# Kernel optimization log

Hardware: AMD Instinct MI355X
Metric: run time of the kernel (lower is better)

The kernel has to match this reference:

```python
import jax, jax.numpy as jnp
import numpy as np
from jax import lax

K = 3  # neighbors, as in torch_geometric.nn.knn_interpolate default
EPS = 1e-16


def knn_interpolate(x, pos_x, pos_y):
    """Interpolate features x defined at pos_x onto query points pos_y.
    x: [Ns, F], pos_x: [Ns, 3], pos_y: [Nq, 3] -> [Nq, F].
    Inverse squared-distance weighting over K nearest neighbors."""
    # squared distances via the |y|^2 + |x|^2 - 2 y.x expansion (no [Nq,Ns,3] temp)
    d2 = (jnp.sum(pos_y * pos_y, -1, keepdims=True)
          + jnp.sum(pos_x * pos_x, -1)[None, :]
          - 2.0 * pos_y @ pos_x.T)                      # [Nq, Ns]
    neg_d2, idx = lax.top_k(-d2, K)                      # [Nq, K]
    w = 1.0 / jnp.clip(-neg_d2, EPS)                     # inverse squared distance
    w = w / jnp.sum(w, -1, keepdims=True)
    return jnp.einsum('qk,qkf->qf', w, x[idx])           # gather + weighted reduce


def mlp(x, W1, b1, W2, b2, W3, b3):
    x = jax.nn.relu(x @ W1 + b1)
    x = jax.nn.relu(x @ W2 + b2)
    return x @ W3 + b3


def setup_inputs() -> dict:
    key = jax.random.key(0)
    ks = jax.random.split(key, 16)
    Nh, Nl, H, O = 16384, 4096, 256, 3
    s = lambda fan: 1.0 / np.sqrt(fan)
    return {
        'emb1':  jax.random.normal(ks[0], (Nh, H), jnp.float32),
        'l_y1':  jax.random.normal(ks[1], (Nl, O), jnp.float32),
        'l_pos1': jax.random.uniform(ks[2], (Nl, 3), jnp.float32),
        'h_pos1': jax.random.uniform(ks[3], (Nh, 3), jnp.float32),
        'emb2':  jax.random.normal(ks[4], (Nh, H), jnp.float32),
        'l_y2':  jax.random.normal(ks[5], (Nl, O), jnp.float32),
        'l_pos2': jax.random.uniform(ks[6], (Nl, 3), jnp.float32),
        'h_pos2': jax.random.uniform(ks[7], (Nh, 3), jnp.float32),
        'W1': jax.random.uniform(ks[8], (H, H), jnp.float32, -s(H), s(H)),
        'b1': jax.random.uniform(ks[9], (H,), jnp.float32, -s(H), s(H)),
        'W2': jax.random.uniform(ks[10], (H, H), jnp.float32, -s(H), s(H)),
        'b2': jax.random.uniform(ks[11], (H,), jnp.float32, -s(H), s(H)),
        'W3': jax.random.uniform(ks[12], (H, O), jnp.float32, -s(H), s(H)),
        'b3': jax.random.uniform(ks[13], (O,), jnp.float32, -s(H), s(H)),
    }


def reference(emb1, l_y1, l_pos1, h_pos1, emb2, l_y2, l_pos2, h_pos2,
              W1, b1, W2, b2, W3, b3):
    x = mlp(emb1 - knn_interpolate(emb2, h_pos2, h_pos1), W1, b1, W2, b2, W3, b3)
    # residual=True branch
    res = knn_interpolate(l_y1 - knn_interpolate(l_y2, l_pos2, l_pos1), l_pos1, h_pos1)
    return x + res
```

## Files before the change

### kernel.cpp

```cpp
#include <hip/hip_runtime.h>
#include <math.h>

#define BIGF 3.0e38f

typedef short  s16x8 __attribute__((ext_vector_type(8)));
typedef float  f32x4 __attribute__((ext_vector_type(4)));

__device__ __forceinline__ unsigned short f2bf(float x) {
  unsigned int b = __float_as_uint(x);
  unsigned int r = b + 0x7FFFu + ((b >> 16) & 1u);
  return (unsigned short)(r >> 16);
}
__device__ __forceinline__ float bf2f(unsigned short h) {
  return __uint_as_float(((unsigned int)h) << 16);
}


__device__ __forceinline__ int cell_clamp(float v, int G) {
  int c = (int)(v * (float)G);
  return min(G - 1, max(0, c));
}

__device__ __forceinline__ void ins3(float d, int id,
                                     float& d0, float& d1, float& d2,
                                     int& i0, int& i1, int& i2) {
  bool l0 = (d < d0) || (d == d0 && id < i0);
  bool l1 = (d < d1) || (d == d1 && id < i1);
  bool l2 = (d < d2) || (d == d2 && id < i2);
  float nd0 = l0 ? d  : d0;  int ni0 = l0 ? id : i0;
  float nd1 = l0 ? d0 : (l1 ? d  : d1);
  int   ni1 = l0 ? i0 : (l1 ? id : i1);
  float nd2 = l1 ? d1 : (l2 ? d  : d2);
  int   ni2 = l1 ? i1 : (l2 ? id : i2);
  d0 = nd0; d1 = nd1; d2 = nd2; i0 = ni0; i1 = ni1; i2 = ni2;
}

__device__ void knn_body(
    int bid,
    const float4* __restrict__ qspts, const int* __restrict__ qsidx, int Nq, int G,
    const int* __restrict__ offs,
    const float4* __restrict__ spts,
    const int* __restrict__ sidx,
    int mode,
    const float* __restrict__ base3,
    const float* __restrict__ feat3,
    float* __restrict__ w_out, int* __restrict__ i_out,
    float* __restrict__ out3)
{
  #pragma clang fp contract(off)
  const int sl = threadIdx.x & 15;
  const int qs = bid * 16 + (threadIdx.x >> 4);
  if (qs >= Nq) return;

  float4 qv = qspts[qs];
  const float qx = qv.x, qy = qv.y, qz = qv.z;
  const float sy = qv.w;
  const int qorig = qsidx[qs];
  const float cs = 1.0f / (float)G;
  const int cx = cell_clamp(qx, G), cy = cell_clamp(qy, G), cz = cell_clamp(qz, G);

  float d0 = BIGF, d1 = BIGF, d2v = BIGF;
  int i0 = -1, i1 = -1, i2 = -1;
  float e0 = BIGF, e1 = BIGF, e2 = BIGF;
  int j0 = -1, j1 = -1, j2 = -1;
  bool done = false;

  #define SCAN()                                                              \
    for (int j = js; j < je; ++j) {                                           \
      float4 s = spts[j];                                                     \
      float p0 = qx * s.x, p1 = qy * s.y, p2 = qz * s.z;                      \
      float dt = (p0 + p1) + p2;                                              \
      float S  = sy + s.w;                                                    \
      float dd = S - 2.0f * dt;                                               \
      ins3(dd, sidx[j], d0, d1, d2v, i0, i1, i2);                             \
    }

  for (int R = 1; R <= G; ++R) {
    if (!done) {
      if (R == 1) {
        if (sl < 9) {
          int dy = sl % 3 - 1, dz = sl / 3 - 1;
          int yy = cy + dy, zz = cz + dz;
          if (yy >= 0 && yy < G && zz >= 0 && zz < G) {
            int xs = max(cx - 1, 0), xe = min(cx + 1, G - 1);
            int base = (zz * G + yy) * G;
            int js = offs[base + xs], je = offs[base + xe + 1];
            SCAN()
          }
        }
      } else {
        const int twoR1 = 2 * R + 1, inner = 2 * R - 1;
        const int nfz = 2 * twoR1;
        const int nfull = nfz + 2 * inner;
        const int half = inner * inner;
        const int nitems = nfull + 2 * half;
        for (int m = sl; m < nitems; m += 16) {
          int dy, dz, js, je;
          if (m < nfull) {
            if (m < nfz) { dz = (m < twoR1) ? -R : R; dy = (m % twoR1) - R; }
            else { int u = m - nfz; dy = (u < inner) ? -R : R; dz = (u % inner) - (R - 1); }
            int yy = cy + dy, zz = cz + dz;
            if (yy < 0 || yy >= G || zz < 0 || zz >= G) continue;
            int xs = max(cx - R, 0), xe = min(cx + R, G - 1);
            int base = (zz * G + yy) * G;
            js = offs[base + xs]; je = offs[base + xe + 1];
          } else {
            int u = m - nfull;
            int xc = (u < half) ? (cx - R) : (cx + R);
            int r2 = (u < half) ? u : u - half;
            dy = r2 % inner - (R - 1); dz = r2 / inner - (R - 1);
            int yy = cy + dy, zz = cz + dz;
            if (xc < 0 || xc >= G || yy < 0 || yy >= G || zz < 0 || zz >= G) continue;
            int c = (zz * G + yy) * G + xc;
            js = offs[c]; je = offs[c + 1];
          }
          SCAN()
        }
      }
    }
    e0 = d0; e1 = d1; e2 = d2v; j0 = i0; j1 = i1; j2 = i2;
    #pragma unroll
    for (int msk = 1; msk < 16; msk <<= 1) {
      float o0 = __shfl_xor(e0, msk), o1 = __shfl_xor(e1, msk), o2 = __shfl_xor(e2, msk);
      int   p0 = __shfl_xor(j0, msk), p1 = __shfl_xor(j1, msk), p2 = __shfl_xor(j2, msk);
      ins3(o0, p0, e0, e1, e2, j0, j1, j2);
      ins3(o1, p1, e0, e1, e2, j0, j1, j2);
      ins3(o2, p2, e0, e1, e2, j0, j1, j2);
    }
    float bnd = (float)R * cs;
    done = done || (e2 <= bnd * bnd - 1e-6f);
    if (__all(done)) break;
  }
  #undef SCAN

  if (sl == 0) {
    float w0 = 1.0f / fmaxf(e0, 1e-16f);
    float w1 = 1.0f / fmaxf(e1, 1e-16f);
    float w2 = 1.0f / fmaxf(e2, 1e-16f);
    float inv = 1.0f / (w0 + w1 + w2);
    w0 *= inv; w1 *= inv; w2 *= inv;
    if (mode == 0) {
      w_out[(size_t)qorig * 3 + 0] = w0; w_out[(size_t)qorig * 3 + 1] = w1; w_out[(size_t)qorig * 3 + 2] = w2;
      i_out[(size_t)qorig * 3 + 0] = j0; i_out[(size_t)qorig * 3 + 1] = j1; i_out[(size_t)qorig * 3 + 2] = j2;
    } else {
      #pragma unroll
      for (int f = 0; f < 3; ++f) {
        float v = w0 * feat3[(size_t)j0 * 3 + f]
                + w1 * feat3[(size_t)j1 * 3 + f]
                + w2 * feat3[(size_t)j2 * 3 + f];
        out3[(size_t)qorig * 3 + f] = (mode == 1) ? (base3[(size_t)qorig * 3 + f] - v) : v;
      }
    }
  }
}

__device__ void build_t_body(
    int bid, const float* __restrict__ emb1, const float* __restrict__ emb2,
    const float* __restrict__ w, const int* __restrict__ idx,
    unsigned short* __restrict__ t_hi, unsigned short* __restrict__ t_lo, int Nq)
{
  int gid = bid * 256 + threadIdx.x;
  int q = gid >> 6, c4 = gid & 63;
  if (q >= Nq) return;
  float w0 = w[(size_t)q * 3 + 0], w1 = w[(size_t)q * 3 + 1], w2 = w[(size_t)q * 3 + 2];
  int i0 = idx[(size_t)q * 3 + 0], i1 = idx[(size_t)q * 3 + 1], i2 = idx[(size_t)q * 3 + 2];
  const float4* e1 = (const float4*)emb1;
  const float4* e2 = (const float4*)emb2;
  float4 a  = e1[(size_t)q * 64 + c4];
  float4 f0 = e2[(size_t)i0 * 64 + c4];
  float4 f1 = e2[(size_t)i1 * 64 + c4];
  float4 f2 = e2[(size_t)i2 * 64 + c4];
  float4 r;
  r.x = a.x - (w0 * f0.x + w1 * f1.x + w2 * f2.x);
  r.y = a.y - (w0 * f0.y + w1 * f1.y + w2 * f2.y);
  r.z = a.z - (w0 * f0.z + w1 * f1.z + w2 * f2.z);
  r.w = a.w - (w0 * f0.w + w1 * f1.w + w2 * f2.w);
  ushort4 h, l;
  h.x = f2bf(r.x); l.x = f2bf(r.x - bf2f(h.x));
  h.y = f2bf(r.y); l.y = f2bf(r.y - bf2f(h.y));
  h.z = f2bf(r.z); l.z = f2bf(r.z - bf2f(h.z));
  h.w = f2bf(r.w); l.w = f2bf(r.w - bf2f(h.w));
  size_t o = (size_t)q * 256 + c4 * 4;
  *(ushort4*)&t_hi[o] = h;
  *(ushort4*)&t_lo[o] = l;
}

__device__ void res_gather_body(
    int bid, const float* __restrict__ wC, const int* __restrict__ idxC,
    const float* __restrict__ diff, float* __restrict__ res, int Nq)
{
  int q = bid * 256 + threadIdx.x;
  if (q >= Nq) return;
  float w0 = wC[(size_t)q * 3 + 0], w1 = wC[(size_t)q * 3 + 1], w2 = wC[(size_t)q * 3 + 2];
  int i0 = idxC[(size_t)q * 3 + 0], i1 = idxC[(size_t)q * 3 + 1], i2 = idxC[(size_t)q * 3 + 2];
  #pragma unroll
  for (int f = 0; f < 3; ++f) {
    res[(size_t)q * 3 + f] = w0 * diff[(size_t)i0 * 3 + f]
                           + w1 * diff[(size_t)i1 * 3 + f]
                           + w2 * diff[(size_t)i2 * 3 + f];
  }
}

__global__ __launch_bounds__(256) void knn_triple_kernel(
    const float4* qspts, const int* qsidx, int Nh, int G1,
    const int* offs1, const float4* spts1, const int* sidx1, float* wA, int* idxA,
    const float4* spts3, const int* sidx3, int Nl, int G2,
    const int* offs2, const float4* spts2, const int* sidx2,
    const float* l_y1, const float* l_y2, float* diff,
    const int* offs3, float* wC, int* idxC)
{
  int g = blockIdx.x / 9, r = blockIdx.x % 9;
  if (r < 4)
    knn_body(g * 4 + r, qspts, qsidx, Nh, G1, offs1, spts1, sidx1, 0,
             nullptr, nullptr, wA, idxA, nullptr);
  else if (r == 4)
    knn_body(g, spts3, sidx3, Nl, G2, offs2, spts2, sidx2, 1,
             l_y1, l_y2, nullptr, nullptr, diff);
  else
    knn_body(g * 4 + (r - 5), qspts, qsidx, Nh, G2, offs3, spts3, sidx3, 0,
             nullptr, nullptr, wC, idxC, nullptr);
}

__global__ __launch_bounds__(256) void bt_gather_kernel(
    const float* emb1, const float* emb2, const float* w, const int* idx,
    unsigned short* t_hi, unsigned short* t_lo, int Nq_bt,
    const float* wC, const int* idxC, const float* diff, float* res, int NqG)
{
  if (blockIdx.x < 64)
    res_gather_body(blockIdx.x, wC, idxC, diff, res, NqG);
  else
    build_t_body(blockIdx.x - 64, emb1, emb2, w, idx, t_hi, t_lo, Nq_bt);
}

__global__ __launch_bounds__(256) void zero_kernel(int* __restrict__ p, int n) {
  int i = blockIdx.x * 256 + threadIdx.x;
  if (i < n) p[i] = 0;
}

__global__ __launch_bounds__(256) void cell_count4_kernel(
    const float* __restrict__ p1, int n1, int g1, int* __restrict__ c1,
    const float* __restrict__ p2, int n2, int g2, int* __restrict__ c2,
    const float* __restrict__ p3, int n3, int g3, int* __restrict__ c3,
    const float* __restrict__ p4, int n4, int g4, int* __restrict__ c4)
{
  int b = blockIdx.x;
  const float* p; int n, G; int* cnt; int i;
  if (b < 64)       { p = p1; n = n1; G = g1; cnt = c1; i = b * 256 + threadIdx.x; }
  else if (b < 80)  { p = p2; n = n2; G = g2; cnt = c2; i = (b - 64) * 256 + threadIdx.x; }
  else if (b < 96)  { p = p3; n = n3; G = g3; cnt = c3; i = (b - 80) * 256 + threadIdx.x; }
  else              { p = p4; n = n4; G = g4; cnt = c4; i = (b - 96) * 256 + threadIdx.x; }
  if (i >= n) return;
  int cx = cell_clamp(p[3 * i],     G);
  int cy = cell_clamp(p[3 * i + 1], G);
  int cz = cell_clamp(p[3 * i + 2], G);
  atomicAdd(&cnt[(cz * G + cy) * G + cx], 1);
}

__global__ __launch_bounds__(256) void prefix4_kernel(
    const int* __restrict__ c1, int* __restrict__ o1, int* __restrict__ u1, int m1,
    const int* __restrict__ c2, int* __restrict__ o2, int* __restrict__ u2, int m2,
    const int* __restrict__ c3, int* __restrict__ o3, int* __restrict__ u3, int m3,
    const int* __restrict__ c4, int* __restrict__ o4, int* __restrict__ u4, int m4)
{
  const int* cnt; int* offs; int* cur; int M;
  if (blockIdx.x == 0)      { cnt = c1; offs = o1; cur = u1; M = m1; }
  else if (blockIdx.x == 1) { cnt = c2; offs = o2; cur = u2; M = m2; }
  else if (blockIdx.x == 2) { cnt = c3; offs = o3; cur = u3; M = m3; }
  else                      { cnt = c4; offs = o4; cur = u4; M = m4; }
  __shared__ int ps[256];
  const int tid = threadIdx.x;
  const int per = (M + 255) >> 8;
  const int base = tid * per;
  int s = 0;
  for (int j = 0; j < per; ++j) if (base + j < M) s += cnt[base + j];
  ps[tid] = s;
  __syncthreads();
  for (int off = 1; off < 256; off <<= 1) {
    int v = (tid >= off) ? ps[tid - off] : 0;
    __syncthreads();
    ps[tid] += v;
    __syncthreads();
  }
  int run = (tid > 0) ? ps[tid - 1] : 0;
  for (int j = 0; j < per; ++j) {
    if (base + j < M) {
      offs[base + j] = run; cur[base + j] = run;
      run += cnt[base + j];
    }
  }
  if (tid == 255) offs[M] = run;
}

__global__ __launch_bounds__(256) void scatter4_kernel(
    const float* __restrict__ p1, int n1, int g1, int* __restrict__ u1, float4* __restrict__ s1, int* __restrict__ x1,
    const float* __restrict__ p2, int n2, int g2, int* __restrict__ u2, float4* __restrict__ s2, int* __restrict__ x2,
    const float* __restrict__ p3, int n3, int g3, int* __restrict__ u3, float4* __restrict__ s3, int* __restrict__ x3,
    const float* __restrict__ p4, int n4, int g4, int* __restrict__ u4, float4* __restrict__ s4, int* __restrict__ x4)
{
  #pragma clang fp contract(off)
  int b = blockIdx.x;
  const float* p; int n, G; int* cur; float4* spts; int* sidx; int i;
  if (b < 64)       { p = p1; n = n1; G = g1; cur = u1; spts = s1; sidx = x1; i = b * 256 + threadIdx.x; }
  else if (b < 80)  { p = p2; n = n2; G = g2; cur = u2; spts = s2; sidx = x2; i = (b - 64) * 256 + threadIdx.x; }
  else if (b < 96)  { p = p3; n = n3; G = g3; cur = u3; spts = s3; sidx = x3; i = (b - 80) * 256 + threadIdx.x; }
  else              { p = p4; n = n4; G = g4; cur = u4; spts = s4; sidx = x4; i = (b - 96) * 256 + threadIdx.x; }
  if (i >= n) return;
  float x = p[3 * i], y = p[3 * i + 1], z = p[3 * i + 2];
  int cx = cell_clamp(x, G), cy = cell_clamp(y, G), cz = cell_clamp(z, G);
  int c = (cz * G + cy) * G + cx;
  int pos = atomicAdd(&cur[c], 1);
  float sx = (x * x + y * y) + z * z;
  spts[pos] = make_float4(x, y, z, sx);
  sidx[pos] = i;
}

__global__ __launch_bounds__(256) void split_wt2_kernel(
    const float* __restrict__ W1, unsigned short* __restrict__ h1T, unsigned short* __restrict__ l1T,
    const float* __restrict__ W2, unsigned short* __restrict__ h2T, unsigned short* __restrict__ l2T)
{
  int b = blockIdx.x;
  const float* W = (b < 256) ? W1 : W2;
  unsigned short* hiT = (b < 256) ? h1T : h2T;
  unsigned short* loT = (b < 256) ? l1T : l2T;
  int id = (b & 255) * 256 + threadIdx.x;
  int k = id >> 8, n = id & 255;
  float x = W[id];
  unsigned short h = f2bf(x);
  unsigned short l = f2bf(x - bf2f(h));
  hiT[n * 256 + k] = h;
  loT[n * 256 + k] = l;
}

__global__ __launch_bounds__(256) void mfma_gemm_kernel(
    const unsigned short* __restrict__ A_hi, const unsigned short* __restrict__ A_lo,
    const unsigned short* __restrict__ BT_hi, const unsigned short* __restrict__ BT_lo,
    const float* __restrict__ bias,
    float* __restrict__ outf,
    unsigned short* __restrict__ out_hi, unsigned short* __restrict__ out_lo,
    int relu, int split_out)
{
  __shared__ unsigned short Bs_hi[64][132];
  __shared__ unsigned short Bs_lo[64][132];
  const int t = threadIdx.x;
  const int d = blockIdx.x;
  const int xcd = d & 7, slot = d >> 3;
  const int lin = xcd * ((int)gridDim.x >> 3) + slot;
  const int row0 = (lin >> 2) * 64;
  const int col0 = (lin & 3) * 64;

  const int l = t & 63, w = t >> 6;
  const int lr = l & 15;
  const int lk = (l >> 4) << 3;
  const unsigned short* arh = A_hi + (size_t)(row0 + w * 16 + lr) * 256;
  const unsigned short* arl = A_lo + (size_t)(row0 + w * 16 + lr) * 256;

  const int sc = t >> 2;
  const int sk = (t & 3) << 5;

  f32x4 acc0 = {0.f,0.f,0.f,0.f}, acc1 = {0.f,0.f,0.f,0.f};
  f32x4 acc2 = {0.f,0.f,0.f,0.f}, acc3 = {0.f,0.f,0.f,0.f};

  #define KSTEP(CT, ACC)                                                      \
    { s16x8 bh = *(const s16x8*)&Bs_hi[CT * 16 + lr][kc + lk];                \
      s16x8 bl = *(const s16x8*)&Bs_lo[CT * 16 + lr][kc + lk];                \
      ACC = __builtin_amdgcn_mfma_f32_16x16x32_bf16(ah, bh, ACC, 0, 0, 0);    \
      ACC = __builtin_amdgcn_mfma_f32_16x16x32_bf16(al, bh, ACC, 0, 0, 0);    \
      ACC = __builtin_amdgcn_mfma_f32_16x16x32_bf16(ah, bl, ACC, 0, 0, 0); }

  for (int half = 0; half < 2; ++half) {
    if (half) __syncthreads();
    {
      const int4* sh = (const int4*)&BT_hi[(size_t)(col0 + sc) * 256 + half * 128 + sk];
      const int4* slo = (const int4*)&BT_lo[(size_t)(col0 + sc) * 256 + half * 128 + sk];
      int4* dh = (int4*)&Bs_hi[sc][sk];
      int4* dl = (int4*)&Bs_lo[sc][sk];
      #pragma unroll
      for (int i = 0; i < 4; ++i) { dh[i] = sh[i]; dl[i] = slo[i]; }
    }
    __syncthreads();
    const int kbase = half * 128;
    #pragma unroll
    for (int kc = 0; kc < 128; kc += 32) {
      s16x8 ah = *(const s16x8*)&arh[kbase + kc + lk];
      s16x8 al = *(const s16x8*)&arl[kbase + kc + lk];
      KSTEP(0, acc0)
      KSTEP(1, acc1)
      KSTEP(2, acc2)
      KSTEP(3, acc3)
    }
  }
  #undef KSTEP

  const int orow = row0 + w * 16 + ((l >> 4) << 2);
  #define EPILOG(CT, ACC)                                                     \
    { int col = col0 + CT * 16 + lr;                                          \
      float bb = bias[col];                                                   \
      _Pragma("unroll")                                                       \
      for (int r = 0; r < 4; ++r) {                                           \
        float v = ACC[r] + bb;                                                \
        if (relu) v = fmaxf(v, 0.0f);                                         \
        size_t o = (size_t)(orow + r) * 256 + col;                            \
        if (split_out) {                                                      \
          unsigned short hh = f2bf(v);                                        \
          out_hi[o] = hh; out_lo[o] = f2bf(v - bf2f(hh));                     \
        } else {                                                              \
          outf[o] = v;                                                        \
        }                                                                     \
      } }
  EPILOG(0, acc0)
  EPILOG(1, acc1)
  EPILOG(2, acc2)
  EPILOG(3, acc3)
  #undef EPILOG
}

__global__ __launch_bounds__(256) void final_kernel(
    const float* __restrict__ h2, const float* __restrict__ W3,
    const float* __restrict__ b3, const float* __restrict__ res,
    float* __restrict__ out, int M)
{
  __shared__ float sW3[768];
  const int tid = threadIdx.x;
  for (int i = tid; i < 768; i += 256) sW3[i] = W3[i];
  __syncthreads();

  const int wave = tid >> 6, lane = tid & 63;
  const int r = blockIdx.x * 4 + wave;
  if (r >= M) return;

  float4 h = ((const float4*)h2)[(size_t)r * 64 + lane];
  const int c = lane * 4;
  float a0 = h.x * sW3[(c + 0) * 3 + 0] + h.y * sW3[(c + 1) * 3 + 0]
           + h.z * sW3[(c + 2) * 3 + 0] + h.w * sW3[(c + 3) * 3 + 0];
  float a1 = h.x * sW3[(c + 0) * 3 + 1] + h.y * sW3[(c + 1) * 3 + 1]
           + h.z * sW3[(c + 2) * 3 + 1] + h.w * sW3[(c + 3) * 3 + 1];
  float a2 = h.x * sW3[(c + 0) * 3 + 2] + h.y * sW3[(c + 1) * 3 + 2]
           + h.z * sW3[(c + 2) * 3 + 2] + h.w * sW3[(c + 3) * 3 + 2];

  #pragma unroll
  for (int off = 32; off; off >>= 1) {
    a0 += __shfl_xor(a0, off);
    a1 += __shfl_xor(a1, off);
    a2 += __shfl_xor(a2, off);
  }
  if (lane == 0) {
    out[(size_t)r * 3 + 0] = a0 + b3[0] + res[(size_t)r * 3 + 0];
    out[(size_t)r * 3 + 1] = a1 + b3[1] + res[(size_t)r * 3 + 1];
    out[(size_t)r * 3 + 2] = a2 + b3[2] + res[(size_t)r * 3 + 2];
  }
}

extern "C" void kernel_launch(void* const* d_in, const int* in_sizes, int n_in,
                              void* d_out, int out_size, void* d_ws, size_t ws_size,
                              hipStream_t stream) {
  (void)in_sizes; (void)n_in; (void)out_size; (void)ws_size;
  const float* emb1   = (const float*)d_in[0];
  const float* l_y1   = (const float*)d_in[1];
  const float* l_pos1 = (const float*)d_in[2];
  const float* h_pos1 = (const float*)d_in[3];
  const float* emb2   = (const float*)d_in[4];
  const float* l_y2   = (const float*)d_in[5];
  const float* l_pos2 = (const float*)d_in[6];
  const float* h_pos2 = (const float*)d_in[7];
  const float* W1     = (const float*)d_in[8];
  const float* b1     = (const float*)d_in[9];
  const float* W2     = (const float*)d_in[10];
  const float* b2     = (const float*)d_in[11];
  const float* W3     = (const float*)d_in[12];
  const float* b3     = (const float*)d_in[13];
  float* out = (float*)d_out;

  const int Nh = 16384, Nl = 4096, H = 256;
  const int G1 = 16, G2 = 10;
  const int M1 = G1 * G1 * G1, M2 = G2 * G2 * G2;

  char* wsp = (char*)d_ws;
  size_t off = 0;
  auto alloc = [&](size_t bytes) -> void* {
    void* p = wsp + off;
    off += (bytes + 255) & ~(size_t)255;
    return p;
  };
  int*            idxA   = (int*)           alloc((size_t)Nh * 3 * 4);
  float*          wA     = (float*)         alloc((size_t)Nh * 3 * 4);
  int*            idxC   = (int*)           alloc((size_t)Nh * 3 * 4);
  float*          wC     = (float*)         alloc((size_t)Nh * 3 * 4);
  unsigned short* t_hi   = (unsigned short*)alloc((size_t)Nh * H * 2);
  unsigned short* t_lo   = (unsigned short*)alloc((size_t)Nh * H * 2);
  unsigned short* h1_hi  = (unsigned short*)alloc((size_t)Nh * H * 2);
  unsigned short* h1_lo  = (unsigned short*)alloc((size_t)Nh * H * 2);
  float*          h2     = (float*)t_hi;
  unsigned short* w1t_hi = (unsigned short*)alloc((size_t)H * H * 2);
  unsigned short* w1t_lo = (unsigned short*)alloc((size_t)H * H * 2);
  unsigned short* w2t_hi = (unsigned short*)alloc((size_t)H * H * 2);
  unsigned short* w2t_lo = (unsigned short*)alloc((size_t)H * H * 2);
  float*          diff   = (float*)         alloc((size_t)Nl * 3 * 4);
  float*          res    = (float*)         alloc((size_t)Nh * 3 * 4);
  int*            cnts   = (int*)           alloc((size_t)(M1 + M2 + M2 + M1) * 4);
  int* cnt1 = cnts, *cnt2 = cnts + M1, *cnt3 = cnts + M1 + M2, *cnt4 = cnts + M1 + 2 * M2;
  int*            offs1  = (int*)           alloc((size_t)(M1 + 1) * 4);
  int*            cur1   = (int*)           alloc((size_t)M1 * 4);
  int*            offs2  = (int*)           alloc((size_t)(M2 + 1) * 4);
  int*            cur2   = (int*)           alloc((size_t)M2 * 4);
  int*            offs3  = (int*)           alloc((size_t)(M2 + 1) * 4);
  int*            cur3   = (int*)           alloc((size_t)M2 * 4);
  int*            offs4  = (int*)           alloc((size_t)(M1 + 1) * 4);
  int*            cur4   = (int*)           alloc((size_t)M1 * 4);
  float4*         spts1  = (float4*)        alloc((size_t)Nh * 16);
  int*            sidx1  = (int*)           alloc((size_t)Nh * 4);
  float4*         spts2  = (float4*)        alloc((size_t)Nl * 16);
  int*            sidx2  = (int*)           alloc((size_t)Nl * 4);
  float4*         spts3  = (float4*)        alloc((size_t)Nl * 16);
  int*            sidx3  = (int*)           alloc((size_t)Nl * 4);
  float4*         qspts  = (float4*)        alloc((size_t)Nh * 16);
  int*            qsidx  = (int*)           alloc((size_t)Nh * 4);

  const int ncnt = M1 + M2 + M2 + M1;
  zero_kernel<<<(ncnt + 255) / 256, 256, 0, stream>>>(cnts, ncnt);
  cell_count4_kernel<<<160, 256, 0, stream>>>(
      h_pos2, Nh, G1, cnt1,  l_pos2, Nl, G2, cnt2,
      l_pos1, Nl, G2, cnt3,  h_pos1, Nh, G1, cnt4);
  prefix4_kernel<<<4, 256, 0, stream>>>(
      cnt1, offs1, cur1, M1,  cnt2, offs2, cur2, M2,
      cnt3, offs3, cur3, M2,  cnt4, offs4, cur4, M1);
  scatter4_kernel<<<160, 256, 0, stream>>>(
      h_pos2, Nh, G1, cur1, spts1, sidx1,
      l_pos2, Nl, G2, cur2, spts2, sidx2,
      l_pos1, Nl, G2, cur3, spts3, sidx3,
      h_pos1, Nh, G1, cur4, qspts, qsidx);
  split_wt2_kernel<<<512, 256, 0, stream>>>(
      W1, w1t_hi, w1t_lo, W2, w2t_hi, w2t_lo);

  knn_triple_kernel<<<2304, 256, 0, stream>>>(
      qspts, qsidx, Nh, G1, offs1, spts1, sidx1, wA, idxA,
      spts3, sidx3, Nl, G2, offs2, spts2, sidx2, l_y1, l_y2, diff,
      offs3, wC, idxC);

  bt_gather_kernel<<<4160, 256, 0, stream>>>(
      emb1, emb2, wA, idxA, t_hi, t_lo, Nh,
      wC, idxC, diff, res, Nh);

  mfma_gemm_kernel<<<(Nh / 64) * 4, 256, 0, stream>>>(
      t_hi, t_lo, w1t_hi, w1t_lo, b1, nullptr, h1_hi, h1_lo, 1, 1);
  mfma_gemm_kernel<<<(Nh / 64) * 4, 256, 0, stream>>>(
      h1_hi, h1_lo, w2t_hi, w2t_lo, b2, h2, nullptr, nullptr, 1, 0);

  final_kernel<<<Nh / 4, 256, 0, stream>>>(h2, W3, b3, res, out, Nh);
}
```

Before: 132.8 us.

## Fuse both high-res KNN searches per query and software-pipeline cell scans

The two KNN searches that share the high-resolution query points (against emb2 positions on grid G1 and l_pos1 on grid G2) now run in one thread group, so query loading and cell setup are shared and the block count drops. The inner cell scan is software-pipelined to prefetch the next point and index while the current one is processed. Separately, the weight bf16 split kernel is merged into the cell-count kernel to save a launch. In exchange, the fused body holds more registers and ties both searches to the slower one's shell loop, which may lower occupancy and cause divergence.

```diff
diff --git a/kernel.cpp b/kernel.cpp
--- a/kernel.cpp
+++ b/kernel.cpp
@@ -35,16 +35,168 @@
   d0 = nd0; d1 = nd1; d2 = nd2; i0 = ni0; i1 = ni1; i2 = ni2;
 }
 
-__device__ void knn_body(
+__device__ __forceinline__ void scan_shell(
+    int R, int sl, int G, int cx, int cy, int cz,
+    const int* __restrict__ offs, const float4* __restrict__ spts,
+    const int* __restrict__ sidx,
+    float qx, float qy, float qz, float sy,
+    float& d0, float& d1, float& d2v, int& i0, int& i1, int& i2)
+{
+  #pragma clang fp contract(off)
+  #define SCANP()                                                             \
+    { int j = js;                                                             \
+      if (j < je) {                                                           \
+        float4 sc = spts[j]; int idc = sidx[j];                               \
+        for (++j; ; ++j) {                                                    \
+          bool more = (j < je);                                               \
+          float4 sn; int idn;                                                 \
+          if (more) { sn = spts[j]; idn = sidx[j]; }                          \
+          float p0 = qx * sc.x, p1 = qy * sc.y, p2 = qz * sc.z;               \
+          float dt = (p0 + p1) + p2;                                          \
+          float S  = sy + sc.w;                                               \
+          float dd = S - 2.0f * dt;                                           \
+          ins3(dd, idc, d0, d1, d2v, i0, i1, i2);                             \
+          if (!more) break;                                                   \
+          sc = sn; idc = idn;                                                 \
+        }                                                                     \
+      } }
+
+  if (R == 1) {
+    if (sl < 9) {
+      int dy = sl % 3 - 1, dz = sl / 3 - 1;
+      int yy = cy + dy, zz = cz + dz;
+      if (yy >= 0 && yy < G && zz >= 0 && zz < G) {
+        int xs = max(cx - 1, 0), xe = min(cx + 1, G - 1);
+        int base = (zz * G + yy) * G;
+        int js = offs[base + xs], je = offs[base + xe + 1];
+        SCANP()
+      }
+    }
+  } else {
+    const int twoR1 = 2 * R + 1, inner = 2 * R - 1;
+    const int nfz = 2 * twoR1;
+    const int nfull = nfz + 2 * inner;
+    const int half = inner * inner;
+    const int nitems = nfull + 2 * half;
+    for (int m = sl; m < nitems; m += 16) {
+      int dy, dz, js, je;
+      if (m < nfull) {
+        if (m < nfz) { dz = (m < twoR1) ? -R : R; dy = (m % twoR1) - R; }
+        else { int u = m - nfz; dy = (u < inner) ? -R : R; dz = (u % inner) - (R - 1); }
+        int yy = cy + dy, zz = cz + dz;
+        if (yy < 0 || yy >= G || zz < 0 || zz >= G) continue;
+        int xs = max(cx - R, 0), xe = min(cx + R, G - 1);
+        int base = (zz * G + yy) * G;
+        js = offs[base + xs]; je = offs[base + xe + 1];
+      } else {
+        int u = m - nfull;
+        int xc = (u < half) ? (cx - R) : (cx + R);
+        int r2 = (u < half) ? u : u - half;
+        dy = r2 % inner - (R - 1); dz = r2 / inner - (R - 1);
+        int yy = cy + dy, zz = cz + dz;
+        if (xc < 0 || xc >= G || yy < 0 || yy >= G || zz < 0 || zz >= G) continue;
+        int c = (zz * G + yy) * G + xc;
+        js = offs[c]; je = offs[c + 1];
+      }
+      SCANP()
+    }
+  }
+  #undef SCANP
+}
+
+#define MERGE16(E0, E1, E2, J0, J1, J2)                                       \
+  { _Pragma("unroll")                                                         \
+    for (int msk = 1; msk < 16; msk <<= 1) {                                  \
+      float o0 = __shfl_xor(E0, msk), o1 = __shfl_xor(E1, msk), o2 = __shfl_xor(E2, msk); \
+      int   p0 = __shfl_xor(J0, msk), p1 = __shfl_xor(J1, msk), p2 = __shfl_xor(J2, msk); \
+      ins3(o0, p0, E0, E1, E2, J0, J1, J2);                                   \
+      ins3(o1, p1, E0, E1, E2, J0, J1, J2);                                   \
+      ins3(o2, p2, E0, E1, E2, J0, J1, J2);                                   \
+    } }
+
+__device__ void knn_dualgrid_body(
+    int bid,
+    const float4* __restrict__ qspts, const int* __restrict__ qsidx, int Nq,
+    int GA, const int* __restrict__ offsA, const float4* __restrict__ sptsA, const int* __restrict__ sidxA,
+    float* __restrict__ wA_out, int* __restrict__ iA_out,
+    int GB, const int* __restrict__ offsB, const float4* __restrict__ sptsB, const int* __restrict__ sidxB,
+    float* __restrict__ wB_out, int* __restrict__ iB_out)
+{
+  #pragma clang fp contract(off)
+  const int sl = threadIdx.x & 15;
+  const int qs = bid * 16 + (threadIdx.x >> 4);
+  if (qs >= Nq) return;
+
+  float4 qv = qspts[qs];
+  const float qx = qv.x, qy = qv.y, qz = qv.z;
+  const float sy = qv.w;
+  const int qorig = qsidx[qs];
+  const float csA = 1.0f / (float)GA, csB = 1.0f / (float)GB;
+  const int cxA = cell_clamp(qx, GA), cyA = cell_clamp(qy, GA), czA = cell_clamp(qz, GA);
+  const int cxB = cell_clamp(qx, GB), cyB = cell_clamp(qy, GB), czB = cell_clamp(qz, GB);
+
+  float a0 = BIGF, a1 = BIGF, a2 = BIGF;  int ia0 = -1, ia1 = -1, ia2 = -1;
+  float b0 = BIGF, b1 = BIGF, b2 = BIGF;  int ib0 = -1, ib1 = -1, ib2 = -1;
+  float eA0 = BIGF, eA1 = BIGF, eA2 = BIGF; int jA0 = -1, jA1 = -1, jA2 = -1;
+  float eB0 = BIGF, eB1 = BIGF, eB2 = BIGF; int jB0 = -1, jB1 = -1, jB2 = -1;
+  bool doneA = false, doneB = false;
+
+  const int Gmax = max(GA, GB);
+  for (int R = 1; R <= Gmax; ++R) {
+    if (!doneA && R <= GA)
+      scan_shell(R, sl, GA, cxA, cyA, czA, offsA, sptsA, sidxA,
+                 qx, qy, qz, sy, a0, a1, a2, ia0, ia1, ia2);
+    if (!doneB && R <= GB)
+      scan_shell(R, sl, GB, cxB, cyB, czB, offsB, sptsB, sidxB,
+                 qx, qy, qz, sy, b0, b1, b2, ib0, ib1, ib2);
+    if (!doneA && R <= GA) {
+      eA0 = a0; eA1 = a1; eA2 = a2; jA0 = ia0; jA1 = ia1; jA2 = ia2;
+      MERGE16(eA0, eA1, eA2, jA0, jA1, jA2)
+      float bnd = (float)R * csA;
+      doneA = (eA2 <= bnd * bnd - 1e-6f) || (R >= GA);
+    }
+    if (!doneB && R <= GB) {
+      eB0 = b0; eB1 = b1; eB2 = b2; jB0 = ib0; jB1 = ib1; jB2 = ib2;
+      MERGE16(eB0, eB1, eB2, jB0, jB1, jB2)
+      float bnd = (float)R * csB;
+      doneB = (eB2 <= bnd * bnd - 1e-6f) || (R >= GB);
+    }
+    if (__all(doneA && doneB)) break;
+  }
+
+  if (sl == 0) {
+    {
+      float w0 = 1.0f / fmaxf(eA0, 1e-16f);
+      float w1 = 1.0f / fmaxf(eA1, 1e-16f);
+      float w2 = 1.0f / fmaxf(eA2, 1e-16f);
+      float inv = 1.0f / (w0 + w1 + w2);
+      wA_out[(size_t)qorig * 3 + 0] = w0 * inv;
+      wA_out[(size_t)qorig * 3 + 1] = w1 * inv;
+      wA_out[(size_t)qorig * 3 + 2] = w2 * inv;
+      iA_out[(size_t)qorig * 3 + 0] = jA0;
+      iA_out[(size_t)qorig * 3 + 1] = jA1;
+      iA_out[(size_t)qorig * 3 + 2] = jA2;
+    }
+    {
+      float w0 = 1.0f / fmaxf(eB0, 1e-16f);
+      float w1 = 1.0f / fmaxf(eB1, 1e-16f);
+      float w2 = 1.0f / fmaxf(eB2, 1e-16f);
+      float inv = 1.0f / (w0 + w1 + w2);
+      wB_out[(size_t)qorig * 3 + 0] = w0 * inv;
+      wB_out[(size_t)qorig * 3 + 1] = w1 * inv;
+      wB_out[(size_t)qorig * 3 + 2] = w2 * inv;
+      iB_out[(size_t)qorig * 3 + 0] = jB0;
+      iB_out[(size_t)qorig * 3 + 1] = jB1;
+      iB_out[(size_t)qorig * 3 + 2] = jB2;
+    }
+  }
+}
+
+__device__ void knn_single_body(
     int bid,
     const float4* __restrict__ qspts, const int* __restrict__ qsidx, int Nq, int G,
-    const int* __restrict__ offs,
-    const float4* __restrict__ spts,
-    const int* __restrict__ sidx,
-    int mode,
-    const float* __restrict__ base3,
-    const float* __restrict__ feat3,
-    float* __restrict__ w_out, int* __restrict__ i_out,
+    const int* __restrict__ offs, const float4* __restrict__ spts, const int* __restrict__ sidx,
+    const float* __restrict__ base3, const float* __restrict__ feat3,
     float* __restrict__ out3)
 {
   #pragma clang fp contract(off)
@@ -65,73 +217,17 @@
   int j0 = -1, j1 = -1, j2 = -1;
   bool done = false;
 
-  #define SCAN()                                                              \
-    for (int j = js; j < je; ++j) {                                           \
-      float4 s = spts[j];                                                     \
-      float p0 = qx * s.x, p1 = qy * s.y, p2 = qz * s.z;                      \
-      float dt = (p0 + p1) + p2;                                              \
-      float S  = sy + s.w;                                                    \
-      float dd = S - 2.0f * dt;                                               \
-      ins3(dd, sidx[j], d0, d1, d2v, i0, i1, i2);                             \
-    }
-
   for (int R = 1; R <= G; ++R) {
     if (!done) {
-      if (R == 1) {
-        if (sl < 9) {
-          int dy = sl % 3 - 1, dz = sl / 3 - 1;
-          int yy = cy + dy, zz = cz + dz;
-          if (yy >= 0 && yy < G && zz >= 0 && zz < G) {
-            int xs = max(cx - 1, 0), xe = min(cx + 1, G - 1);
-            int base = (zz * G + yy) * G;
-            int js = offs[base + xs], je = offs[base + xe + 1];
-            SCAN()
-          }
-        }
-      } else {
-        const int twoR1 = 2 * R + 1, inner = 2 * R - 1;
-        const int nfz = 2 * twoR1;
-        const int nfull = nfz + 2 * inner;
-        const int half = inner * inner;
-        const int nitems = nfull + 2 * half;
-        for (int m = sl; m < nitems; m += 16) {
-          int dy, dz, js, je;
-          if (m < nfull) {
-            if (m < nfz) { dz = (m < twoR1) ? -R : R; dy = (m % twoR1) - R; }
-            else { int u = m - nfz; dy = (u < inner) ? -R : R; dz = (u % inner) - (R - 1); }
-            int yy = cy + dy, zz = cz + dz;
-            if (yy < 0 || yy >= G || zz < 0 || zz >= G) continue;
-            int xs = max(cx - R, 0), xe = min(cx + R, G - 1);
-            int base = (zz * G + yy) * G;
-            js = offs[base + xs]; je = offs[base + xe + 1];
-          } else {
-            int u = m - nfull;
-            int xc = (u < half) ? (cx - R) : (cx + R);
-            int r2 = (u < half) ? u : u - half;
-            dy = r2 % inner - (R - 1); dz = r2 / inner - (R - 1);
-            int yy = cy + dy, zz = cz + dz;
-            if (xc < 0 || xc >= G || yy < 0 || yy >= G || zz < 0 || zz >= G) continue;
-            int c = (zz * G + yy) * G + xc;
-            js = offs[c]; je = offs[c + 1];
-          }
-          SCAN()
-        }
-      }
-    }
-    e0 = d0; e1 = d1; e2 = d2v; j0 = i0; j1 = i1; j2 = i2;
-    #pragma unroll
-    for (int msk = 1; msk < 16; msk <<= 1) {
-      float o0 = __shfl_xor(e0, msk), o1 = __shfl_xor(e1, msk), o2 = __shfl_xor(e2, msk);
-      int   p0 = __shfl_xor(j0, msk), p1 = __shfl_xor(j1, msk), p2 = __shfl_xor(j2, msk);
-      ins3(o0, p0, e0, e1, e2, j0, j1, j2);
-      ins3(o1, p1, e0, e1, e2, j0, j1, j2);
-      ins3(o2, p2, e0, e1, e2, j0, j1, j2);
-    }
-    float bnd = (float)R * cs;
-    done = done || (e2 <= bnd * bnd - 1e-6f);
+      scan_shell(R, sl, G, cx, cy, cz, offs, spts, sidx,
+                 qx, qy, qz, sy, d0, d1, d2v, i0, i1, i2);
+      e0 = d0; e1 = d1; e2 = d2v; j0 = i0; j1 = i1; j2 = i2;
+      MERGE16(e0, e1, e2, j0, j1, j2)
+      float bnd = (float)R * cs;
+      done = (e2 <= bnd * bnd - 1e-6f) || (R >= G);
+    }
     if (__all(done)) break;
   }
-  #undef SCAN
 
   if (sl == 0) {
     float w0 = 1.0f / fmaxf(e0, 1e-16f);
@@ -139,17 +235,12 @@
     float w2 = 1.0f / fmaxf(e2, 1e-16f);
     float inv = 1.0f / (w0 + w1 + w2);
     w0 *= inv; w1 *= inv; w2 *= inv;
-    if (mode == 0) {
-      w_out[(size_t)qorig * 3 + 0] = w0; w_out[(size_t)qorig * 3 + 1] = w1; w_out[(size_t)qorig * 3 + 2] = w2;
-      i_out[(size_t)qorig * 3 + 0] = j0; i_out[(size_t)qorig * 3 + 1] = j1; i_out[(size_t)qorig * 3 + 2] = j2;
-    } else {
-      #pragma unroll
-      for (int f = 0; f < 3; ++f) {
-        float v = w0 * feat3[(size_t)j0 * 3 + f]
-                + w1 * feat3[(size_t)j1 * 3 + f]
-                + w2 * feat3[(size_t)j2 * 3 + f];
-        out3[(size_t)qorig * 3 + f] = (mode == 1) ? (base3[(size_t)qorig * 3 + f] - v) : v;
-      }
+    #pragma unroll
+    for (int f = 0; f < 3; ++f) {
+      float v = w0 * feat3[(size_t)j0 * 3 + f]
+              + w1 * feat3[(size_t)j1 * 3 + f]
+              + w2 * feat3[(size_t)j2 * 3 + f];
+      out3[(size_t)qorig * 3 + f] = base3[(size_t)qorig * 3 + f] - v;
     }
   }
 }
@@ -201,24 +292,21 @@
   }
 }
 
-__global__ __launch_bounds__(256) void knn_triple_kernel(
-    const float4* qspts, const int* qsidx, int Nh, int G1,
-    const int* offs1, const float4* spts1, const int* sidx1, float* wA, int* idxA,
-    const float4* spts3, const int* sidx3, int Nl, int G2,
-    const int* offs2, const float4* spts2, const int* sidx2,
-    const float* l_y1, const float* l_y2, float* diff,
-    const int* offs3, float* wC, int* idxC)
-{
-  int g = blockIdx.x / 9, r = blockIdx.x % 9;
+__global__ __launch_bounds__(256) void knn_fused_kernel(
+    const float4* qspts, const int* qsidx, int Nh,
+    int G1, const int* offs1, const float4* spts1, const int* sidx1, float* wA, int* idxA,
+    int G2, const int* offs3, const float4* spts3, const int* sidx3, float* wC, int* idxC,
+    int Nl, const int* offs2, const float4* spts2, const int* sidx2,
+    const float* l_y1, const float* l_y2, float* diff)
+{
+  int g = blockIdx.x / 5, r = blockIdx.x % 5;
   if (r < 4)
-    knn_body(g * 4 + r, qspts, qsidx, Nh, G1, offs1, spts1, sidx1, 0,
-             nullptr, nullptr, wA, idxA, nullptr);
-  else if (r == 4)
-    knn_body(g, spts3, sidx3, Nl, G2, offs2, spts2, sidx2, 1,
-             l_y1, l_y2, nullptr, nullptr, diff);
+    knn_dualgrid_body(g * 4 + r, qspts, qsidx, Nh,
+                      G1, offs1, spts1, sidx1, wA, idxA,
+                      G2, offs3, spts3, sidx3, wC, idxC);
   else
-    knn_body(g * 4 + (r - 5), qspts, qsidx, Nh, G2, offs3, spts3, sidx3, 0,
-             nullptr, nullptr, wC, idxC, nullptr);
+    knn_single_body(g, spts3, sidx3, Nl, G2, offs2, spts2, sidx2,
+                    l_y1, l_y2, diff);
 }
 
 __global__ __launch_bounds__(256) void bt_gather_kernel(
@@ -237,13 +325,29 @@
   if (i < n) p[i] = 0;
 }
 
-__global__ __launch_bounds__(256) void cell_count4_kernel(
+__global__ __launch_bounds__(256) void count_split_kernel(
     const float* __restrict__ p1, int n1, int g1, int* __restrict__ c1,
     const float* __restrict__ p2, int n2, int g2, int* __restrict__ c2,
     const float* __restrict__ p3, int n3, int g3, int* __restrict__ c3,
-    const float* __restrict__ p4, int n4, int g4, int* __restrict__ c4)
+    const float* __restrict__ p4, int n4, int g4, int* __restrict__ c4,
+    const float* __restrict__ W1, unsigned short* __restrict__ h1T, unsigned short* __restrict__ l1T,
+    const float* __restrict__ W2, unsigned short* __restrict__ h2T, unsigned short* __restrict__ l2T)
 {
   int b = blockIdx.x;
+  if (b >= 160) {
+    int sb = b - 160;
+    const float* W = (sb < 256) ? W1 : W2;
+    unsigned short* hiT = (sb < 256) ? h1T : h2T;
+    unsigned short* loT = (sb < 256) ? l1T : l2T;
+    int id = (sb & 255) * 256 + threadIdx.x;
+    int k = id >> 8, n = id & 255;
+    float x = W[id];
+    unsigned short h = f2bf(x);
+    unsigned short l = f2bf(x - bf2f(h));
+    hiT[n * 256 + k] = h;
+    loT[n * 256 + k] = l;
+    return;
+  }
   const float* p; int n, G; int* cnt; int i;
   if (b < 64)       { p = p1; n = n1; G = g1; cnt = c1; i = b * 256 + threadIdx.x; }
   else if (b < 80)  { p = p2; n = n2; G = g2; cnt = c2; i = (b - 64) * 256 + threadIdx.x; }
@@ -312,23 +416,6 @@
   float sx = (x * x + y * y) + z * z;
   spts[pos] = make_float4(x, y, z, sx);
   sidx[pos] = i;
-}
-
-__global__ __launch_bounds__(256) void split_wt2_kernel(
-    const float* __restrict__ W1, unsigned short* __restrict__ h1T, unsigned short* __restrict__ l1T,
-    const float* __restrict__ W2, unsigned short* __restrict__ h2T, unsigned short* __restrict__ l2T)
-{
-  int b = blockIdx.x;
-  const float* W = (b < 256) ? W1 : W2;
-  unsigned short* hiT = (b < 256) ? h1T : h2T;
-  unsigned short* loT = (b < 256) ? l1T : l2T;
-  int id = (b & 255) * 256 + threadIdx.x;
-  int k = id >> 8, n = id & 255;
-  float x = W[id];
-  unsigned short h = f2bf(x);
-  unsigned short l = f2bf(x - bf2f(h));
-  hiT[n * 256 + k] = h;
-  loT[n * 256 + k] = l;
 }
 
 __global__ __launch_bounds__(256) void mfma_gemm_kernel(
@@ -517,9 +604,10 @@
 
   const int ncnt = M1 + M2 + M2 + M1;
   zero_kernel<<<(ncnt + 255) / 256, 256, 0, stream>>>(cnts, ncnt);
-  cell_count4_kernel<<<160, 256, 0, stream>>>(
+  count_split_kernel<<<672, 256, 0, stream>>>(
       h_pos2, Nh, G1, cnt1,  l_pos2, Nl, G2, cnt2,
-      l_pos1, Nl, G2, cnt3,  h_pos1, Nh, G1, cnt4);
+      l_pos1, Nl, G2, cnt3,  h_pos1, Nh, G1, cnt4,
+      W1, w1t_hi, w1t_lo, W2, w2t_hi, w2t_lo);
   prefix4_kernel<<<4, 256, 0, stream>>>(
       cnt1, offs1, cur1, M1,  cnt2, offs2, cur2, M2,
       cnt3, offs3, cur3, M2,  cnt4, offs4, cur4, M1);
@@ -528,13 +616,12 @@
       l_pos2, Nl, G2, cur2, spts2, sidx2,
       l_pos1, Nl, G2, cur3, spts3, sidx3,
       h_pos1, Nh, G1, cur4, qspts, qsidx);
-  split_wt2_kernel<<<512, 256, 0, stream>>>(
-      W1, w1t_hi, w1t_lo, W2, w2t_hi, w2t_lo);
-
-  knn_triple_kernel<<<2304, 256, 0, stream>>>(
-      qspts, qsidx, Nh, G1, offs1, spts1, sidx1, wA, idxA,
-      spts3, sidx3, Nl, G2, offs2, spts2, sidx2, l_y1, l_y2, diff,
-      offs3, wC, idxC);
+
+  knn_fused_kernel<<<1280, 256, 0, stream>>>(
+      qspts, qsidx, Nh,
+      G1, offs1, spts1, sidx1, wA, idxA,
+      G2, offs3, spts3, sidx3, wC, idxC,
+      Nl, offs2, spts2, sidx2, l_y1, l_y2, diff);
 
   bt_gather_kernel<<<4160, 256, 0, stream>>>(
       emb1, emb2, wA, idxA, t_hi, t_lo, Nh,
```

After: 127.8 us. 3.8% less time.
